# Performance work log

Hardware: AMD Instinct MI355X
Metric: run time of the kernel (lower is better)

Reference implementation:

```python
import jax, jax.numpy as jnp
import numpy as np

N = 50000
E = 1600000
IN_C = 32
OUT_C = 32
OUT_SIZE = 1


def setup_inputs() -> dict:
    key = jax.random.key(0)
    ks = jax.random.split(key, 16)
    x = jax.random.normal(ks[0], (N, IN_C), dtype=jnp.float32)
    edge_index = jax.random.randint(ks[1], (2, E), 0, N, dtype=jnp.int64)

    def glorot(k, shape):
        lim = float(np.sqrt(6.0 / (shape[0] + shape[1])))
        return jax.random.uniform(k, shape, jnp.float32, -lim, lim)

    params = {
        # GCNConv weights for gates z, r, h: [in, out] and bias [out]
        'Wz_c': glorot(ks[2], (IN_C, OUT_C)), 'bz_c': jnp.zeros((OUT_C,), jnp.float32),
        'Wr_c': glorot(ks[3], (IN_C, OUT_C)), 'br_c': jnp.zeros((OUT_C,), jnp.float32),
        'Wh_c': glorot(ks[4], (IN_C, OUT_C)), 'bh_c': jnp.zeros((OUT_C,), jnp.float32),
        # GRU linear layers: [2*out, out] and bias [out]
        'Wz_l': glorot(ks[5], (2 * OUT_C, OUT_C)), 'bz_l': jnp.zeros((OUT_C,), jnp.float32),
        'Wr_l': glorot(ks[6], (2 * OUT_C, OUT_C)), 'br_l': jnp.zeros((OUT_C,), jnp.float32),
        'Wh_l': glorot(ks[7], (2 * OUT_C, OUT_C)), 'bh_l': jnp.zeros((OUT_C,), jnp.float32),
        # final readout Linear(out_channels, output_size)
        'W_lin': glorot(ks[8], (OUT_C, OUT_SIZE)), 'b_lin': jnp.zeros((OUT_SIZE,), jnp.float32),
    }
    return {'x': x, 'edge_index': edge_index, **params}


def _gcn_conv(x, W, b, src, dst, n_nodes):
    """GCNConv with add_self_loops=False, symmetric normalization."""
    h = x @ W  # [N, out]
    ones = jnp.ones((src.shape[0],), h.dtype)
    deg = jax.ops.segment_sum(ones, dst, num_segments=n_nodes)  # in-degree at targets
    dinv = jnp.where(deg > 0, jax.lax.rsqrt(jnp.maximum(deg, 1e-12)), 0.0)
    norm = dinv[src] * dinv[dst]  # [E]
    msg = h[src] * norm[:, None]  # gather + scale
    agg = jax.ops.segment_sum(msg, dst, num_segments=n_nodes)  # scatter-add
    return agg + b


def reference(x, edge_index, Wz_c, bz_c, Wr_c, br_c, Wh_c, bh_c,
              Wz_l, bz_l, Wr_l, br_l, Wh_l, bh_l, W_lin, b_lin):
    src, dst = edge_index[0], edge_index[1]
    n = x.shape[0]
    H = jnp.zeros((n, OUT_C), x.dtype)  # H=None -> zeros

    Z = jax.nn.sigmoid(jnp.concatenate([_gcn_conv(x, Wz_c, bz_c, src, dst, n), H], axis=1) @ Wz_l + bz_l)
    R = jax.nn.sigmoid(jnp.concatenate([_gcn_conv(x, Wr_c, br_c, src, dst, n), H], axis=1) @ Wr_l + br_l)
    H_tilde = jnp.tanh(jnp.concatenate([_gcn_conv(x, Wh_c, bh_c, src, dst, n), H * R], axis=1) @ Wh_l + bh_l)
    H = Z * H + (1.0 - Z) * H_tilde

    h = jax.nn.relu(H)
    return h @ W_lin + b_lin  # [N, output_size]
```

## Files before the change

kernel.cpp:

```cpp
#include <hip/hip_runtime.h>
#include <hip/hip_fp16.h>
#include <math.h>

#define NN 50000
#define NE 1600000
#define ELLW 80
#define SHN 6250
#define XH_WORDS 800000

#define NBIN 400
#define BINW 125
#define NBLK 782
#define HDRW 404
#define MAGIC125 34359739u

#define NEED_A ((4000000ull + 800000 + 800000 + 50000 + 2112) * 4)
#define NEED_B ((4000000ull + 800000 + 50000 + 2112) * 4)

struct h2x2 { __half2 a, b; };

__global__ __launch_bounds__(512) void bucket_kernel(
        const int* __restrict__ ei,
        unsigned int* __restrict__ bkt, unsigned int* __restrict__ hdr,
        const float* __restrict__ Wz_c, const float* __restrict__ bz_c,
        const float* __restrict__ Wh_c, const float* __restrict__ bh_c,
        const float* __restrict__ Wz_l, const float* __restrict__ bz_l,
        const float* __restrict__ Wh_l, const float* __restrict__ bh_l,
        float* __restrict__ Mz, float* __restrict__ Mh,
        float* __restrict__ cz, float* __restrict__ ch,
        const float* __restrict__ x, __half2* __restrict__ xh) {
    int t = threadIdx.x;
    int b = blockIdx.x;
    if (b >= NBLK) {
        if (b == NBLK) {
            for (int p = t; p < 1024; p += 512) {
                int i = p >> 5, j = p & 31;
                float az = 0.0f, ah = 0.0f;
                for (int k = 0; k < 32; ++k) {
                    az += Wz_c[i * 32 + k] * Wz_l[k * 32 + j];
                    ah += Wh_c[i * 32 + k] * Wh_l[k * 32 + j];
                }
                Mz[p] = az;
                Mh[p] = ah;
            }
            if (t < 32) {
                int j = t;
                float sz = bz_l[j], sh = bh_l[j];
                for (int k = 0; k < 32; ++k) {
                    sz += bz_c[k] * Wz_l[k * 32 + j];
                    sh += bh_c[k] * Wh_l[k * 32 + j];
                }
                cz[j] = sz;
                ch[j] = sh;
            }
        } else if (xh) {
            int idx = (b - NBLK - 1) * 512 + t;
            int stride = (gridDim.x - NBLK - 1) * 512;
            const float2* x2 = (const float2*)x;
            for (int i = idx; i < XH_WORDS; i += stride) {
                float2 v = x2[i];
                xh[i] = __floats2half2_rn(v.x, v.y);
            }
        }
        return;
    }
    __shared__ unsigned int lcnt[NBIN];
    __shared__ unsigned int lstart[NBIN];
    __shared__ unsigned int loff[NBIN];
    __shared__ alignas(16) unsigned int stage[2048];
    for (int i = t; i < NBIN; i += 512) lcnt[i] = 0u;
    __syncthreads();
    int i4 = b * 512 + t;
    bool valid = (i4 < NE / 4);
    int4 s4 = make_int4(0, 0, 0, 0), d4 = make_int4(0, 0, 0, 0);
    if (valid) {
        s4 = ((const int4*)ei)[i4];
        d4 = ((const int4*)(ei + NE))[i4];
#define CNT_E(dd, ss)                                                       \
        if ((unsigned)(dd) < NN && (unsigned)(ss) < NN)                     \
            atomicAdd(&lcnt[__umulhi((unsigned)(dd), MAGIC125)], 1u);
        CNT_E(d4.x, s4.x) CNT_E(d4.y, s4.y) CNT_E(d4.z, s4.z) CNT_E(d4.w, s4.w)
#undef CNT_E
    }
    __syncthreads();
    if (t < NBIN) loff[t] = lcnt[t];
    __syncthreads();
    for (int off = 1; off < NBIN; off <<= 1) {
        unsigned v = 0;
        if (t < NBIN && t >= off) v = loff[t - off];
        __syncthreads();
        if (t < NBIN) loff[t] += v;
        __syncthreads();
    }
    if (t < NBIN) {
        lstart[t] = loff[t] - lcnt[t];
        hdr[b * HDRW + t] = loff[t] - lcnt[t];
    }
    if (t == 0) hdr[b * HDRW + NBIN] = loff[NBIN - 1];
    __syncthreads();
    if (t < NBIN) loff[t] = lstart[t];
    __syncthreads();
    if (valid) {
#define SC_E(dd, ss)                                                        \
        if ((unsigned)(dd) < NN && (unsigned)(ss) < NN) {                   \
            unsigned bn = __umulhi((unsigned)(dd), MAGIC125);               \
            unsigned p = atomicAdd(&loff[bn], 1u);                          \
            stage[p] = ((unsigned)(dd) << 16) | (unsigned)(ss);             \
        }
        SC_E(d4.x, s4.x) SC_E(d4.y, s4.y) SC_E(d4.z, s4.z) SC_E(d4.w, s4.w)
#undef SC_E
    }
    __syncthreads();
    ((uint4*)bkt)[b * 512 + t] = ((const uint4*)stage)[t];
}

__global__ __launch_bounds__(256) void build_ell_kernel(const unsigned int* __restrict__ bkt,
                                                        const unsigned int* __restrict__ hdr,
                                                        unsigned int* __restrict__ cnt,
                                                        float* __restrict__ dinv,
                                                        unsigned short* __restrict__ ell) {
    __shared__ unsigned int lcnt[BINW];
    __shared__ alignas(16) unsigned short stage[BINW * ELLW];
    int t = threadIdx.x;
    int blk = blockIdx.x;
    int bin = (blk & 7) * 50 + (blk >> 3);
    int nbase = bin * BINW;
    for (int i = t; i < BINW; i += 256) lcnt[i] = 0u;
    __syncthreads();
    for (int b = t; b < NBLK; b += 256) {
        unsigned o0 = hdr[b * HDRW + bin];
        unsigned o1 = hdr[b * HDRW + bin + 1];
        const unsigned int* bp = bkt + b * 2048;
        for (unsigned i = o0; i < o1; ++i) {
            unsigned v = bp[i];
            unsigned ld = (v >> 16) - (unsigned)nbase;
            unsigned p = atomicAdd(&lcnt[ld], 1u);
            if (p < ELLW) stage[ld * ELLW + p] = (unsigned short)(v & 0xffffu);
        }
    }
    __syncthreads();
    const uint2* st2 = (const uint2*)stage;
    uint2* ell2 = (uint2*)(ell + (size_t)nbase * ELLW);
    for (int i = t; i < BINW * ELLW / 4; i += 256) ell2[i] = st2[i];
    for (int i = t; i < BINW; i += 256) {
        unsigned d = lcnt[i];
        cnt[nbase + i] = d;
        dinv[nbase + i] = d ? rsqrtf((float)d) : 0.0f;
    }
}

template <int USE_H>
__global__ __launch_bounds__(256) void gather_node_kernel(const unsigned short* __restrict__ ell,
                                                          const unsigned int* __restrict__ cnt,
                                                          const float* __restrict__ dinv,
                                                          const float* __restrict__ x,
                                                          const h2x2* __restrict__ xh,
                                                          const float* __restrict__ Mz,
                                                          const float* __restrict__ Mh,
                                                          const float* __restrict__ cz,
                                                          const float* __restrict__ ch,
                                                          const float* __restrict__ Wlin,
                                                          const float* __restrict__ blin,
                                                          float* __restrict__ out) {
    __shared__ float sMz[1024], sMh[1024], scz[32], sch[32], sw[32];
    __shared__ float xs[8][32];
    int t = threadIdx.x;
    for (int i = t; i < 1024; i += 256) { sMz[i] = Mz[i]; sMh[i] = Mh[i]; }
    if (t < 32) { scz[t] = cz[t]; sch[t] = ch[t]; sw[t] = Wlin[t]; }
    __syncthreads();

    int l    = t & 63;
    int slot = t >> 5;
    int q    = l & 31;
    int hb   = l & 32;
    int shard = blockIdx.x & 7;
    int grp   = blockIdx.x >> 3;
    int ns = grp * 8 + slot;
    if (ns >= SHN) return;
    int n = shard * SHN + ns;

    int base = n * ELLW;
    int len0 = (int)cnt[n];
    float dn = len0 ? rsqrtf((float)len0) : 0.0f;
    int len = len0 > ELLW ? ELLW : len0;
    int lenW = max(len, __shfl_xor(len, 32));

    const float4* x4 = (const float4*)x;
    int es = q >> 3;
    int k  = q & 7;
    float4 acc = make_float4(0.f, 0.f, 0.f, 0.f);

    for (int c0 = 0; c0 < lenW; c0 += 32) {
        int m = len - c0; if (m > 32) m = 32;
        int mw = lenW - c0; if (mw > 32) mw = 32;
        int s = 0; float wgt = 0.0f;
        if (q < m) { s = (int)ell[base + c0 + q]; wgt = dinv[s]; }
#define SW(j0) { int sl = hb + (j0) + es; int sj = __shfl(s, sl); float wj = __shfl(wgt, sl); \
                 if (USE_H) {                                                              \
                     h2x2 hv = xh[sj * 8 + k];                                             \
                     float2 f0 = __half22float2(hv.a), f1 = __half22float2(hv.b);          \
                     acc.x += f0.x * wj; acc.y += f0.y * wj;                               \
                     acc.z += f1.x * wj; acc.w += f1.y * wj;                               \
                 } else {                                                                  \
                     float4 v = x4[sj * 8 + k];                                            \
                     acc.x += v.x * wj; acc.y += v.y * wj;                                 \
                     acc.z += v.z * wj; acc.w += v.w * wj;                                 \
                 } }
        SW(0) SW(4)
        if (mw > 8)  { SW(8)  SW(12) }
        if (mw > 16) { SW(16) SW(20) }
        if (mw > 24) { SW(24) SW(28) }
#undef SW
    }
    #pragma unroll
    for (int mm = 8; mm <= 16; mm <<= 1) {
        acc.x += __shfl_xor(acc.x, mm);
        acc.y += __shfl_xor(acc.y, mm);
        acc.z += __shfl_xor(acc.z, mm);
        acc.w += __shfl_xor(acc.w, mm);
    }
    if (es == 0) {
        float4* xs4 = (float4*)&xs[slot][0];
        xs4[k] = make_float4(acc.x * dn, acc.y * dn, acc.z * dn, acc.w * dn);
    }

    int j = q;
    float az = scz[j];
    float ah = sch[j];
    #pragma unroll
    for (int i = 0; i < 32; ++i) {
        float v = xs[slot][i];
        az += v * sMz[i * 32 + j];
        ah += v * sMh[i * 32 + j];
    }
    float z  = 1.0f / (1.0f + __expf(-az));
    float ht = tanhf(ah);
    float hv = (1.0f - z) * ht;
    hv = hv > 0.0f ? hv : 0.0f;
    float val = hv * sw[j];
    val += __shfl_xor(val, 1);
    val += __shfl_xor(val, 2);
    val += __shfl_xor(val, 4);
    val += __shfl_xor(val, 8);
    val += __shfl_xor(val, 16);
    if (q == 0) out[n] = val + blin[0];
}

extern "C" void kernel_launch(void* const* d_in, const int* in_sizes, int n_in,
                              void* d_out, int out_size, void* d_ws, size_t ws_size,
                              hipStream_t stream) {
    const float* x    = (const float*)d_in[0];
    const int*   ei   = (const int*)d_in[1];
    const float* Wz_c = (const float*)d_in[2];
    const float* bz_c = (const float*)d_in[3];
    const float* Wh_c = (const float*)d_in[6];
    const float* bh_c = (const float*)d_in[7];
    const float* Wz_l = (const float*)d_in[8];
    const float* bz_l = (const float*)d_in[9];
    const float* Wh_l = (const float*)d_in[12];
    const float* bh_l = (const float*)d_in[13];
    const float* Wlin = (const float*)d_in[14];
    const float* blin = (const float*)d_in[15];
    float* out = (float*)d_out;
    float* ws = (float*)d_ws;

    int use_h = (ws_size >= NEED_A) ? 1 : 0;

    unsigned short* ell16 = (unsigned short*)(ws);
    unsigned int*   cnt   = (unsigned int*)(ws + 2000000);
    __half2*        xh    = use_h ? (__half2*)(ws + 2050000) : nullptr;
    float*          dinv  = ws + 2050000 + (use_h ? XH_WORDS : 0);
    float*          Mz    = dinv + NN;
    float*          Mh    = Mz + 1024;
    float*          cz    = Mh + 1024;
    float*          ch    = cz + 32;
    unsigned int*   bkt   = (unsigned int*)(ch + 32);
    unsigned int*   hdr   = bkt + (size_t)NBLK * 2048;

    const int k1_grid   = NBLK + 1 + (use_h ? 225 : 0);
    const int build_grid = NBIN;
    const int node_grid  = 8 * ((SHN + 7) / 8);

    bucket_kernel<<<k1_grid, 512, 0, stream>>>(ei, bkt, hdr,
                                               Wz_c, bz_c, Wh_c, bh_c,
                                               Wz_l, bz_l, Wh_l, bh_l,
                                               Mz, Mh, cz, ch, x, xh);
    build_ell_kernel<<<build_grid, 256, 0, stream>>>(bkt, hdr, cnt, dinv, ell16);
    if (use_h) {
        gather_node_kernel<1><<<node_grid, 256, 0, stream>>>(
            ell16, cnt, dinv, x, (const h2x2*)xh, Mz, Mh, cz, ch, Wlin, blin, out);
    } else {
        gather_node_kernel<0><<<node_grid, 256, 0, stream>>>(
            ell16, cnt, dinv, x, (const h2x2*)nullptr, Mz, Mh, cz, ch, Wlin, blin, out);
    }
}
```

Before: 152.2 us.

## Pre-scale half-precision features by dinv in build kernel, drop per-edge weight gather

Moves the fp32-to-fp16 conversion of x from the bucket kernel into the ELL build kernel, where each node's features are pre-multiplied by its dinv. The gather kernel then no longer loads dinv[src] per edge or shuffles a weight, and padded lanes point at a zeroed sentinel row instead of being masked. This removes a dependent random load per edge in the hot gather, at the cost of serializing the conversion after bucketing instead of overlapping it with that kernel.

```diff
diff --git a/kernel.cpp b/kernel.cpp
--- a/kernel.cpp
+++ b/kernel.cpp
@@ -6,7 +6,7 @@
 #define NE 1600000
 #define ELLW 80
 #define SHN 6250
-#define XH_WORDS 800000
+#define XH_WORDS 800016
 
 #define NBIN 400
 #define BINW 125
@@ -28,40 +28,31 @@
         const float* __restrict__ Wh_l, const float* __restrict__ bh_l,
         float* __restrict__ Mz, float* __restrict__ Mh,
         float* __restrict__ cz, float* __restrict__ ch,
-        const float* __restrict__ x, __half2* __restrict__ xh) {
+        __half2* __restrict__ xh) {
     int t = threadIdx.x;
     int b = blockIdx.x;
     if (b >= NBLK) {
-        if (b == NBLK) {
-            for (int p = t; p < 1024; p += 512) {
-                int i = p >> 5, j = p & 31;
-                float az = 0.0f, ah = 0.0f;
-                for (int k = 0; k < 32; ++k) {
-                    az += Wz_c[i * 32 + k] * Wz_l[k * 32 + j];
-                    ah += Wh_c[i * 32 + k] * Wh_l[k * 32 + j];
-                }
-                Mz[p] = az;
-                Mh[p] = ah;
+        for (int p = t; p < 1024; p += 512) {
+            int i = p >> 5, j = p & 31;
+            float az = 0.0f, ah = 0.0f;
+            for (int k = 0; k < 32; ++k) {
+                az += Wz_c[i * 32 + k] * Wz_l[k * 32 + j];
+                ah += Wh_c[i * 32 + k] * Wh_l[k * 32 + j];
             }
-            if (t < 32) {
-                int j = t;
-                float sz = bz_l[j], sh = bh_l[j];
-                for (int k = 0; k < 32; ++k) {
-                    sz += bz_c[k] * Wz_l[k * 32 + j];
-                    sh += bh_c[k] * Wh_l[k * 32 + j];
-                }
-                cz[j] = sz;
-                ch[j] = sh;
+            Mz[p] = az;
+            Mh[p] = ah;
+        }
+        if (t < 32) {
+            int j = t;
+            float sz = bz_l[j], sh = bh_l[j];
+            for (int k = 0; k < 32; ++k) {
+                sz += bz_c[k] * Wz_l[k * 32 + j];
+                sh += bh_c[k] * Wh_l[k * 32 + j];
             }
-        } else if (xh) {
-            int idx = (b - NBLK - 1) * 512 + t;
-            int stride = (gridDim.x - NBLK - 1) * 512;
-            const float2* x2 = (const float2*)x;
-            for (int i = idx; i < XH_WORDS; i += stride) {
-                float2 v = x2[i];
-                xh[i] = __floats2half2_rn(v.x, v.y);
-            }
-        }
+            cz[j] = sz;
+            ch[j] = sh;
+        }
+        if (xh && t < 16) ((unsigned int*)xh)[NN * 16 + t] = 0u;
         return;
     }
     __shared__ unsigned int lcnt[NBIN];
@@ -118,8 +109,11 @@
                                                         const unsigned int* __restrict__ hdr,
                                                         unsigned int* __restrict__ cnt,
                                                         float* __restrict__ dinv,
-                                                        unsigned short* __restrict__ ell) {
+                                                        unsigned short* __restrict__ ell,
+                                                        const float* __restrict__ x,
+                                                        __half2* __restrict__ xh) {
     __shared__ unsigned int lcnt[BINW];
+    __shared__ float ldinv[BINW];
     __shared__ alignas(16) unsigned short stage[BINW * ELLW];
     int t = threadIdx.x;
     int blk = blockIdx.x;
@@ -144,8 +138,20 @@
     for (int i = t; i < BINW * ELLW / 4; i += 256) ell2[i] = st2[i];
     for (int i = t; i < BINW; i += 256) {
         unsigned d = lcnt[i];
+        float dv = d ? rsqrtf((float)d) : 0.0f;
         cnt[nbase + i] = d;
-        dinv[nbase + i] = d ? rsqrtf((float)d) : 0.0f;
+        dinv[nbase + i] = dv;
+        ldinv[i] = dv;
+    }
+    if (xh) {
+        __syncthreads();
+        const float2* x2 = (const float2*)x;
+        for (int p = t; p < BINW * 16; p += 256) {
+            int i = p >> 4, c = p & 15;
+            float2 v = x2[(size_t)(nbase + i) * 16 + c];
+            float dv = ldinv[i];
+            xh[(size_t)(nbase + i) * 16 + c] = __floats2half2_rn(v.x * dv, v.y * dv);
+        }
     }
 }
 
@@ -193,15 +199,21 @@
     for (int c0 = 0; c0 < lenW; c0 += 32) {
         int m = len - c0; if (m > 32) m = 32;
         int mw = lenW - c0; if (mw > 32) mw = 32;
-        int s = 0; float wgt = 0.0f;
-        if (q < m) { s = (int)ell[base + c0 + q]; wgt = dinv[s]; }
-#define SW(j0) { int sl = hb + (j0) + es; int sj = __shfl(s, sl); float wj = __shfl(wgt, sl); \
+        int s; float wgt = 0.0f;
+        if (USE_H) {
+            s = (q < m) ? (int)ell[base + c0 + q] : NN;
+        } else {
+            s = 0;
+            if (q < m) { s = (int)ell[base + c0 + q]; wgt = dinv[s]; }
+        }
+#define SW(j0) { int sl = hb + (j0) + es; int sj = __shfl(s, sl);                          \
                  if (USE_H) {                                                              \
                      h2x2 hv = xh[sj * 8 + k];                                             \
                      float2 f0 = __half22float2(hv.a), f1 = __half22float2(hv.b);          \
-                     acc.x += f0.x * wj; acc.y += f0.y * wj;                               \
-                     acc.z += f1.x * wj; acc.w += f1.y * wj;                               \
+                     acc.x += f0.x; acc.y += f0.y;                                         \
+                     acc.z += f1.x; acc.w += f1.y;                                         \
                  } else {                                                                  \
+                     float wj = __shfl(wgt, sl);                                           \
                      float4 v = x4[sj * 8 + k];                                            \
                      acc.x += v.x * wj; acc.y += v.y * wj;                                 \
                      acc.z += v.z * wj; acc.w += v.w * wj;                                 \
@@ -277,15 +289,15 @@
     unsigned int*   bkt   = (unsigned int*)(ch + 32);
     unsigned int*   hdr   = bkt + (size_t)NBLK * 2048;
 
-    const int k1_grid   = NBLK + 1 + (use_h ? 225 : 0);
+    const int k1_grid    = NBLK + 1;
     const int build_grid = NBIN;
     const int node_grid  = 8 * ((SHN + 7) / 8);
 
     bucket_kernel<<<k1_grid, 512, 0, stream>>>(ei, bkt, hdr,
                                                Wz_c, bz_c, Wh_c, bh_c,
                                                Wz_l, bz_l, Wh_l, bh_l,
-                                               Mz, Mh, cz, ch, x, xh);
-    build_ell_kernel<<<build_grid, 256, 0, stream>>>(bkt, hdr, cnt, dinv, ell16);
+                                               Mz, Mh, cz, ch, xh);
+    build_ell_kernel<<<build_grid, 256, 0, stream>>>(bkt, hdr, cnt, dinv, ell16, x, xh);
     if (use_h) {
         gather_node_kernel<1><<<node_grid, 256, 0, stream>>>(
             ell16, cnt, dinv, x, (const h2x2*)xh, Mz, Mh, cz, ch, Wlin, blin, out);
```

Result: no change. 149.4 us (-1.8%).
